# Optimization experiments

Measured on AMD Instinct MI355X. Metric: run time of the kernel, lower is better.

The kernel has to match this reference:

```python
import jax, jax.numpy as jnp
import numpy as np

D_MODEL = 1024


def setup_inputs() -> dict:
    key = jax.random.key(0)
    ks = jax.random.split(key, 7)
    s = 1.0 / np.sqrt(D_MODEL)
    return {
        "x": jax.random.normal(ks[0], (4, 4096, D_MODEL), dtype=jnp.float32),
        "Wq": jax.random.normal(ks[1], (D_MODEL, D_MODEL), dtype=jnp.float32) * s,
        "bq": jax.random.normal(ks[2], (D_MODEL,), dtype=jnp.float32) * s,
        "Wk": jax.random.normal(ks[3], (D_MODEL, D_MODEL), dtype=jnp.float32) * s,
        "bk": jax.random.normal(ks[4], (D_MODEL,), dtype=jnp.float32) * s,
        "Wv": jax.random.normal(ks[5], (D_MODEL, D_MODEL), dtype=jnp.float32) * s,
        "bv": jax.random.normal(ks[6], (D_MODEL,), dtype=jnp.float32) * s,
    }


def reference(x, Wq, bq, Wk, bk, Wv, bv):
    # nn.Linear: y = x @ W.T + b
    Q = jnp.einsum("bsd,ed->bse", x, Wq) + bq  # [B,S,D]
    K = jnp.einsum("bsd,ed->bse", x, Wk) + bk
    V = jnp.einsum("bsd,ed->bse", x, Wv) + bv
    scale = 1.0 / jnp.sqrt(jnp.asarray(x.shape[-1], dtype=x.dtype))
    KV = jnp.einsum("bsd,bse->bde", K, V) * scale  # [B,D,D]
    E = jnp.einsum("bsd,bde->bse", Q, KV)  # [B,S,D]
    return E
```

## Files before the change

### kernel.cpp

```cpp
#include <hip/hip_runtime.h>
#include <hip/hip_fp16.h>


#define BATCH 4
#define SEQ   4096
#define DM    1024

typedef _Float16 h8 __attribute__((ext_vector_type(8)));
typedef _Float16 h4 __attribute__((ext_vector_type(4)));
typedef float    f4 __attribute__((ext_vector_type(4)));

__device__ inline void gload_lds16(const _Float16* g, _Float16* l) {
    __builtin_amdgcn_global_load_lds(
        (const __attribute__((address_space(1))) void*)g,
        (__attribute__((address_space(3))) void*)l,
        16, 0, 0);
}

__device__ inline int xcd_swz(int bid, int grid) {
    const int q = grid >> 3;
    return (bid & 7) * q + (bid >> 3);
}

__device__ inline float doth(const _Float16* wr, const float* v, int lane) {
    float s = 0.f;
    #pragma unroll
    for (int i = 0; i < 2; ++i) {
        const int k = i * 512 + lane * 8;
        h8 wv = *(const h8*)&wr[k];
        f4 v0 = *(const f4*)&v[k];
        f4 v1 = *(const f4*)&v[k + 4];
        s += (float)wv[0] * v0.x + (float)wv[1] * v0.y +
             (float)wv[2] * v0.z + (float)wv[3] * v0.w +
             (float)wv[4] * v1.x + (float)wv[5] * v1.y +
             (float)wv[6] * v1.z + (float)wv[7] * v1.w;
    }
    return s;
}
__device__ inline float dotf(const float* a, const float* b, int lane) {
    float s = 0.f;
    #pragma unroll
    for (int i = 0; i < 4; ++i) {
        const int k = i * 256 + lane * 4;
        f4 x = *(const f4*)&a[k];
        f4 y = *(const f4*)&b[k];
        s += x.x * y.x + x.y * y.y + x.z * y.z + x.w * y.w;
    }
    return s;
}
__device__ inline float wred(float s) {
    #pragma unroll
    for (int off = 32; off; off >>= 1) s += __shfl_down(s, off);
    return s;
}

__global__ __launch_bounds__(256) void cvt_x(
    const float* __restrict__ src, _Float16* __restrict__ dstT,
    _Float16* __restrict__ dstRM, float* __restrict__ xs, int R, int C)
{
    __shared__ float tile[64][65];
    __shared__ float red[4][64];
    const long zoff = (long)blockIdx.z * R * C;
    src += zoff; dstT += zoff; dstRM += zoff;
    const int r0 = blockIdx.y * 64;
    const int c0 = blockIdx.x * 64;
    const int t  = threadIdx.x;
    const int tr = t >> 4;
    const int tc = (t & 15) * 4;
    #pragma unroll
    for (int i = 0; i < 4; ++i) {
        const int r = tr + i * 16;
        f4 v = *(const f4*)&src[(long)(r0 + r) * C + c0 + tc];
        tile[r][tc + 0] = v.x; tile[r][tc + 1] = v.y;
        tile[r][tc + 2] = v.z; tile[r][tc + 3] = v.w;
        h4 h = { (_Float16)v.x, (_Float16)v.y, (_Float16)v.z, (_Float16)v.w };
        *(h4*)&dstRM[(long)(r0 + r) * C + c0 + tc] = h;
    }
    __syncthreads();
    #pragma unroll
    for (int i = 0; i < 4; ++i) {
        const int c = tr + i * 16;
        h4 h = { (_Float16)tile[tc + 0][c], (_Float16)tile[tc + 1][c],
                 (_Float16)tile[tc + 2][c], (_Float16)tile[tc + 3][c] };
        *(h4*)&dstT[(long)(c0 + c) * R + r0 + tc] = h;
    }
    {
        const int cc = t & 63;
        const int rb = (t >> 6) * 16;
        float ps = 0.f;
        #pragma unroll
        for (int r = 0; r < 16; ++r) ps += tile[rb + r][cc];
        red[t >> 6][cc] = ps;
    }
    __syncthreads();
    if (t < 64)
        atomicAdd(&xs[blockIdx.z * DM + c0 + t],
                  red[0][t] + red[1][t] + red[2][t] + red[3][t]);
}

__global__ __launch_bounds__(256) void wcvt(
    const float* __restrict__ Wq, const float* __restrict__ Wk,
    const float* __restrict__ Wv,
    _Float16* __restrict__ Wqt, _Float16* __restrict__ Wkt,
    _Float16* __restrict__ Wkh, _Float16* __restrict__ Wvh)
{
    __shared__ float tile[64][65];
    const int z = blockIdx.z;
    const float* src = z == 0 ? Wq : (z == 1 ? Wk : Wv);
    _Float16* dstT  = z == 0 ? Wqt : (z == 1 ? Wkt : nullptr);
    _Float16* dstRM = z == 0 ? nullptr : (z == 1 ? Wkh : Wvh);
    const int r0 = blockIdx.y * 64;
    const int c0 = blockIdx.x * 64;
    const int t  = threadIdx.x;
    const int tr = t >> 4;
    const int tc = (t & 15) * 4;
    #pragma unroll
    for (int i = 0; i < 4; ++i) {
        const int r = tr + i * 16;
        f4 v = *(const f4*)&src[(long)(r0 + r) * DM + c0 + tc];
        tile[r][tc + 0] = v.x; tile[r][tc + 1] = v.y;
        tile[r][tc + 2] = v.z; tile[r][tc + 3] = v.w;
        if (dstRM) {
            h4 h = { (_Float16)v.x, (_Float16)v.y, (_Float16)v.z, (_Float16)v.w };
            *(h4*)&dstRM[(long)(r0 + r) * DM + c0 + tc] = h;
        }
    }
    __syncthreads();
    if (dstT) {
        #pragma unroll
        for (int i = 0; i < 4; ++i) {
            const int c = tr + i * 16;
            h4 h = { (_Float16)tile[tc + 0][c], (_Float16)tile[tc + 1][c],
                     (_Float16)tile[tc + 2][c], (_Float16)tile[tc + 3][c] };
            *(h4*)&dstT[(long)(c0 + c) * DM + r0 + tc] = h;
        }
    }
}

__global__ __launch_bounds__(256) void gemv_misc(
    const _Float16* __restrict__ Wvh, const _Float16* __restrict__ Wkh,
    const _Float16* __restrict__ Wqt, const _Float16* __restrict__ Wkt,
    const float* __restrict__ xs, const float* __restrict__ bv,
    const float* __restrict__ bk, const float* __restrict__ bq,
    float* __restrict__ vecs)
{
    const int gw   = blockIdx.x * 4 + (threadIdx.x >> 6);
    const int lane = threadIdx.x & 63;
    const _Float16* wr;
    const float* v;
    if (gw < 4096)      { wr = Wvh + (long)(gw & 1023) * DM; v = xs + (gw >> 10) * DM; }
    else if (gw < 8192) { wr = Wkh + (long)(gw & 1023) * DM; v = xs + ((gw - 4096) >> 10) * DM; }
    else if (gw < 9216) { wr = Wqt + (long)(gw - 8192) * DM; v = bk; }
    else                { wr = Wkt + (long)(gw - 9216) * DM; v = bq; }
    float s = wred(doth(wr, v, lane));
    if (lane == 0) {
        if (gw < 4096) s += (float)SEQ * bv[gw & 1023];
        vecs[gw] = s;
    }
}

__global__ __launch_bounds__(256) void gemv_qw(
    const _Float16* __restrict__ Wqt, const float* __restrict__ w,
    const float* __restrict__ bq, const float* __restrict__ bk,
    float* __restrict__ qw, float* __restrict__ sv)
{
    const int gw   = blockIdx.x * 4 + (threadIdx.x >> 6);
    const int lane = threadIdx.x & 63;
    if (gw < 4096) {
        float s = wred(doth(Wqt + (long)(gw & 1023) * DM, w + (gw >> 10) * DM, lane));
        if (lane == 0) qw[gw] = s;
    } else if (gw == 4096) {
        float s = wred(dotf(bq, bk, lane));
        if (lane == 0) sv[0] = s;
    } else if (gw <= 4100) {
        float s = wred(dotf(bq, w + (gw - 4097) * DM, lane));
        if (lane == 0) sv[1 + (gw - 4097)] = s;
    }
}

__global__ __launch_bounds__(256) void gemv_cv(
    const _Float16* __restrict__ Ph, const float* __restrict__ kb,
    const float* __restrict__ u2, const float* __restrict__ bv,
    const float* __restrict__ sv, float* __restrict__ cv)
{
    const int gw   = blockIdx.x * 4 + (threadIdx.x >> 6);
    const int lane = threadIdx.x & 63;
    const int b    = gw >> 10;
    const int e    = gw & 1023;
    float s = wred(doth(Ph + (long)b * DM * DM + (long)e * DM, kb, lane));
    if (lane == 0)
        cv[gw] = s + (sv[0] * u2[gw] + sv[1 + b] * bv[e]) * 0.03125f;
}

__global__ __launch_bounds__(256) void reduce_tri(
    const _Float16* __restrict__ parts, _Float16* __restrict__ Gh)
{
    __shared__ _Float16 lds[64][72];
    const int bid = blockIdx.x;
    const int job = bid >> 4;
    const int ch  = bid & 15;
    const int b   = job / 10;
    const int p   = job - b * 10;
    const int ti  = p >= 6 ? 3 : (p >= 3 ? 2 : (p >= 1 ? 1 : 0));
    const int tj  = p - ((ti * (ti + 1)) >> 1);
    const int li  = (ch >> 2) * 64;
    const int lj  = (ch & 3) * 64;
    const int t   = threadIdx.x;
    const int c8  = (t & 7) * 8;
    const long DD_ = (long)DM * DM;

    h8 o[2];
    #pragma unroll
    for (int h = 0; h < 2; ++h) {
        const int r = (t >> 3) + h * 32;
        float a[8] = {};
        #pragma unroll
        for (int s = 0; s < 6; ++s) {
            const _Float16* src = parts + ((long)(job * 6 + s) << 16);
            h8 v = *(const h8*)&src[(li + r) * 256 + lj + c8];
            #pragma unroll
            for (int j = 0; j < 8; ++j) a[j] += (float)v[j];
        }
        #pragma unroll
        for (int j = 0; j < 8; ++j) o[h][j] = (_Float16)(a[j] * 0.03125f);
        *(h8*)&Gh[b * DD_ + (long)(ti * 256 + li + r) * DM + tj * 256 + lj + c8] = o[h];
        *(h8*)&lds[r][c8] = o[h];
    }
    if (ti != tj) {
        __syncthreads();
        #pragma unroll
        for (int h = 0; h < 2; ++h) {
            const int r = (t >> 3) + h * 32;
            h8 m;
            #pragma unroll
            for (int j = 0; j < 8; ++j) m[j] = lds[c8 + j][r];
            *(h8*)&Gh[b * DD_ + (long)(tj * 256 + lj + r) * DM + ti * 256 + li + c8] = m;
        }
    }
}

template<typename OutT, int BIAS, int TRI>
__global__ __launch_bounds__(512, 1) void gemm8p(
    const _Float16* __restrict__ A, const _Float16* __restrict__ B,
    OutT* __restrict__ C,
    int K, int lda, int ldb, int ldc, int tilesX, int perZ,
    long aZ, long bZ, long cZ, int sk, long aK, long bK,
    const float* __restrict__ bc1, long bc1Z, float alpha)
{
    __shared__ _Float16 lds[2 * 32768];

    const int L = xcd_swz(blockIdx.x, gridDim.x);
    int tileM, tileN, cTileM, cTileN, NT;
    const float* pc1 = nullptr;
    if (TRI) {
        const int job = L / 6;
        const int s   = L - job * 6;
        const int b   = job / 10;
        const int p   = job - b * 10;
        const int ti  = p >= 6 ? 3 : (p >= 3 ? 2 : (p >= 1 ? 1 : 0));
        const int tj  = p - ((ti * (ti + 1)) >> 1);
        const int kOff = s < 4 ? s * 704 : 2816 + (s - 4) * 640;
        NT = s < 4 ? 11 : 10;
        A += (long)b * aZ + kOff;
        B += (long)b * aZ + kOff;
        C += (long)(job * 6 + s) * cZ;
        tileM = ti * 256; tileN = tj * 256;
        cTileM = 0; cTileN = 0;
    } else {
        const int z  = L / perZ;
        const int r0 = L - z * perZ;
        const int zb = z / sk;
        const int zk = z - zb * sk;
        A += (long)zb * aZ + (long)zk * aK;
        B += (long)zb * bZ + (long)zk * bK;
        C += (long)z * cZ;
        if (BIAS == 1) pc1 = bc1 + (long)zb * bc1Z;
        tileM = (r0 / tilesX) * 256;
        tileN = (r0 % tilesX) * 256;
        cTileM = tileM; cTileN = tileN;
        NT = K >> 6;
    }

    const int tid  = threadIdx.x;
    const int lane = tid & 63;
    const int wave = tid >> 6;
    const int wr   = wave >> 2;
    const int wc   = wave & 3;
    const int la   = lane & 15;
    const int kg   = lane >> 4;

    auto stageA = [&](int buf, int mq, int kt) {
        _Float16* dst = &lds[buf * 32768 + mq * 8192];
        const int k0 = kt * 64;
        #pragma unroll
        for (int i = 0; i < 2; ++i) {
            const int U = i * 512 + tid;
            const int R = U >> 3, s = U & 7;
            const int gr = tileM + (R >> 6) * 128 + mq * 64 + (R & 63);
            gload_lds16(&A[(long)gr * lda + k0 + ((s ^ (R & 7)) << 3)], dst + U * 8);
        }
    };
    auto stageB = [&](int buf, int nq, int kt) {
        _Float16* dst = &lds[buf * 32768 + 16384 + nq * 8192];
        const int k0 = kt * 64;
        #pragma unroll
        for (int i = 0; i < 2; ++i) {
            const int U = i * 512 + tid;
            const int R = U >> 3, s = U & 7;
            const int gn = tileN + (R >> 5) * 64 + nq * 32 + (R & 31);
            gload_lds16(&B[(long)gn * ldb + k0 + ((s ^ (R & 7)) << 3)], dst + U * 8);
        }
    };

    f4 acc[8][4] = {};
    h8 af[4][2];
    h8 bf[2][2][2];

    auto readA = [&](int buf, int mq) {
        const _Float16* Ab = &lds[buf * 32768 + mq * 8192];
        #pragma unroll
        for (int mi = 0; mi < 4; ++mi)
            #pragma unroll
            for (int kk = 0; kk < 2; ++kk) {
                const int R = wr * 64 + mi * 16 + la;
                const int s = kk * 4 + kg;
                af[mi][kk] = *(const h8*)&Ab[R * 64 + ((s ^ (R & 7)) << 3)];
            }
    };
    auto readB = [&](int buf, int nq) {
        const _Float16* Bb = &lds[buf * 32768 + 16384 + nq * 8192];
        #pragma unroll
        for (int ni = 0; ni < 2; ++ni)
            #pragma unroll
            for (int kk = 0; kk < 2; ++kk) {
                const int R = wc * 32 + ni * 16 + la;
                const int s = kk * 4 + kg;
                bf[nq][ni][kk] = *(const h8*)&Bb[R * 64 + ((s ^ (R & 7)) << 3)];
            }
    };
    auto mfmaQ = [&](int mq, int nq) {
        __builtin_amdgcn_s_setprio(1);
        #pragma unroll
        for (int mi = 0; mi < 4; ++mi)
            #pragma unroll
            for (int ni = 0; ni < 2; ++ni)
                #pragma unroll
                for (int kk = 0; kk < 2; ++kk)
                    acc[mq * 4 + mi][nq * 2 + ni] =
                        __builtin_amdgcn_mfma_f32_16x16x32_f16(
                            af[mi][kk], bf[nq][ni][kk],
                            acc[mq * 4 + mi][nq * 2 + ni], 0, 0, 0);
        __builtin_amdgcn_s_setprio(0);
    };

    stageA(0, 0, 0); stageA(0, 1, 0); stageB(0, 0, 0); stageB(0, 1, 0);
    if (NT > 1) {
        stageA(1, 0, 1); stageB(1, 0, 1);
        asm volatile("s_waitcnt vmcnt(4)" ::: "memory");
    } else {
        asm volatile("s_waitcnt vmcnt(0)" ::: "memory");
    }
    __builtin_amdgcn_sched_barrier(0);
    __builtin_amdgcn_s_barrier();

    for (int j = 0; j < NT; ++j) {
        const int buf = j & 1;
        readA(buf, 0); readB(buf, 0);
        if (j + 1 < NT) stageA(buf ^ 1, 1, j + 1);
        asm volatile("s_waitcnt lgkmcnt(8)" ::: "memory");
        __builtin_amdgcn_s_barrier();
        asm volatile("s_waitcnt lgkmcnt(0)" ::: "memory");
        __builtin_amdgcn_sched_barrier(0);
        mfmaQ(0, 0);
        __builtin_amdgcn_s_barrier();
        readB(buf, 1);
        if (j + 1 < NT) stageB(buf ^ 1, 1, j + 1);
        __builtin_amdgcn_s_barrier();
        asm volatile("s_waitcnt lgkmcnt(0)" ::: "memory");
        __builtin_amdgcn_sched_barrier(0);
        mfmaQ(0, 1);
        __builtin_amdgcn_s_barrier();
        readA(buf, 1);
        if (j + 2 < NT) stageA(buf, 0, j + 2);
        __builtin_amdgcn_s_barrier();
        asm volatile("s_waitcnt lgkmcnt(0)" ::: "memory");
        __builtin_amdgcn_sched_barrier(0);
        mfmaQ(1, 0);
        __builtin_amdgcn_s_barrier();
        if (j + 2 < NT) stageB(buf, 0, j + 2);
        __builtin_amdgcn_s_barrier();
        mfmaQ(1, 1);
        if (j + 2 < NT) {
            asm volatile("s_waitcnt vmcnt(4)" ::: "memory");
        } else if (j + 1 < NT) {
            asm volatile("s_waitcnt vmcnt(0)" ::: "memory");
        }
        __builtin_amdgcn_sched_barrier(0);
        __builtin_amdgcn_s_barrier();
    }

    #pragma unroll
    for (int mf = 0; mf < 8; ++mf) {
        #pragma unroll
        for (int nf = 0; nf < 4; ++nf) {
            const int col = cTileN + wc * 64 + nf * 16 + la;
            #pragma unroll
            for (int jj = 0; jj < 4; ++jj) {
                const int row = cTileM + wr * 128 + mf * 16 + kg * 4 + jj;
                float v = acc[mf][nf][jj] * alpha;
                if (BIAS == 1) v += pc1[col];
                C[(long)row * ldc + col] = (OutT)v;
            }
        }
    }
}

template<int BIAS>
__global__ __launch_bounds__(256) void gemm64(
    const _Float16* __restrict__ A, const _Float16* __restrict__ B,
    _Float16* __restrict__ C,
    const _Float16* __restrict__ A2, const _Float16* __restrict__ B2,
    _Float16* __restrict__ C2, int zSplit,
    int K, int lda, int ldb, int ldc, int tilesX, int perZ,
    long aZ, long bZ, long cZ,
    const float* __restrict__ bc1, long bc1Z,
    const float* __restrict__ br1, long br1Z,
    const float* __restrict__ bc2, long bc2Z,
    const float* __restrict__ br2, long br2Z,
    float alpha, float beta)
{
    __shared__ _Float16 As[64 * 64];
    __shared__ _Float16 Bs[64 * 64];

    const int L  = xcd_swz(blockIdx.x, gridDim.x);
    int z        = L / perZ;
    const int r0 = L - z * perZ;
    if (z >= zSplit) { A = A2; B = B2; C = C2; z = 0; }
    A += (long)z * aZ;
    B += (long)z * bZ;
    C += (long)z * cZ;
    const float* pc1 = nullptr; const float* pr1 = nullptr;
    const float* pc2 = nullptr; const float* pr2 = nullptr;
    if (BIAS == 3) {
        pc1 = bc1 + (long)z * bc1Z; pr1 = br1 + (long)z * br1Z;
        pc2 = bc2 + (long)z * bc2Z; pr2 = br2 + (long)z * br2Z;
    }

    const int tileM = (r0 / tilesX) * 64;
    const int tileN = (r0 % tilesX) * 64;
    const int tid   = threadIdx.x;
    const int lane  = tid & 63;
    const int wave  = tid >> 6;
    const int wm    = (wave >> 1) * 32;
    const int wn    = (wave & 1) * 32;
    const int srow  = tid >> 3;
    const int sslot = tid & 7;

    f4 acc[2][2] = {};
    const int arow = lane & 15;
    const int kg   = lane >> 4;

    for (int k0 = 0; k0 < K; k0 += 64) {
        #pragma unroll
        for (int i = 0; i < 2; ++i) {
            const int row   = i * 32 + srow;
            const int gslot = sslot ^ (row & 7);
            gload_lds16(&A[(long)(tileM + row) * lda + k0 + gslot * 8],
                        &As[row * 64 + sslot * 8]);
            gload_lds16(&B[(long)(tileN + row) * ldb + k0 + gslot * 8],
                        &Bs[row * 64 + sslot * 8]);
        }
        __syncthreads();

        #pragma unroll
        for (int kk = 0; kk < 64; kk += 32) {
            h8 af[2], bf[2];
            #pragma unroll
            for (int m = 0; m < 2; ++m) {
                const int rr   = wm + m * 16 + arow;
                const int slot = (kk >> 3) + kg;
                af[m] = *(const h8*)&As[rr * 64 + ((slot ^ (rr & 7)) << 3)];
            }
            #pragma unroll
            for (int n = 0; n < 2; ++n) {
                const int rr   = wn + n * 16 + arow;
                const int slot = (kk >> 3) + kg;
                bf[n] = *(const h8*)&Bs[rr * 64 + ((slot ^ (rr & 7)) << 3)];
            }
            #pragma unroll
            for (int m = 0; m < 2; ++m)
                #pragma unroll
                for (int n = 0; n < 2; ++n)
                    acc[m][n] = __builtin_amdgcn_mfma_f32_16x16x32_f16(
                        af[m], bf[n], acc[m][n], 0, 0, 0);
        }
        __syncthreads();
    }

    #pragma unroll
    for (int m = 0; m < 2; ++m) {
        #pragma unroll
        for (int n = 0; n < 2; ++n) {
            const int col = tileN + wn + n * 16 + arow;
            #pragma unroll
            for (int j = 0; j < 4; ++j) {
                const int row = tileM + wm + m * 16 + (lane >> 4) * 4 + j;
                float v = acc[m][n][j] * alpha;
                if (BIAS == 3) v += beta * (pc1[col] * pr1[row] + pc2[col] * pr2[row]);
                C[(long)row * ldc + col] = (_Float16)v;
            }
        }
    }
}

extern "C" void kernel_launch(void* const* d_in, const int* in_sizes, int n_in,
                              void* d_out, int out_size, void* d_ws, size_t ws_size,
                              hipStream_t stream)
{
    const float* x  = (const float*)d_in[0];
    const float* Wq = (const float*)d_in[1];
    const float* bq = (const float*)d_in[2];
    const float* Wk = (const float*)d_in[3];
    const float* bk = (const float*)d_in[4];
    const float* Wv = (const float*)d_in[5];
    const float* bv = (const float*)d_in[6];
    float* out = (float*)d_out;

    const long DD = (long)DM * DM;
    const long DS = (long)DM * SEQ;
    const long MB = 1024l * 1024;

    char* base = (char*)d_ws;
    _Float16* xh   = (_Float16*)base;
    _Float16* xt   = (_Float16*)(base + 32 * MB);
    _Float16* Gh   = xt;
    _Float16* Ph   = (_Float16*)(base + 40 * MB);
    _Float16* Rth  = (_Float16*)(base + 48 * MB);
    _Float16* Wqt  = (_Float16*)(base + 64 * MB);
    _Float16* Wkh  = (_Float16*)(base + 66 * MB);
    _Float16* Wvh  = (_Float16*)(base + 68 * MB);
    _Float16* Wkt  = (_Float16*)(base + 70 * MB);
    _Float16* Mh   = (_Float16*)(base + 72 * MB);
    float*    vecs = (float*)(base + 74 * MB);
    float*    u2   = vecs;
    float*    w    = vecs + 4096;
    float*    qk   = vecs + 8192;
    float*    kb   = vecs + 9216;
    float*    xs   = vecs + 10240;
    float*    qw   = vecs + 14336;
    float*    cv   = vecs + 18432;
    float*    sv   = vecs + 22528;
    _Float16* parts = (_Float16*)d_out;

    hipMemsetAsync(xs, 0, BATCH * DM * sizeof(float), stream);

    cvt_x<<<dim3(16, 64, 4), 256, 0, stream>>>(x, xt, xh, xs, SEQ, DM);
    wcvt<<<dim3(16, 16, 3), 256, 0, stream>>>(Wq, Wk, Wv, Wqt, Wkt, Wkh, Wvh);

    gemv_misc<<<2560, 256, 0, stream>>>(Wvh, Wkh, Wqt, Wkt, xs, bv, bk, bq, vecs);

    gemv_qw<<<1026, 256, 0, stream>>>(Wqt, w, bq, bk, qw, sv);

    gemm8p<_Float16, 0, 1><<<240, 512, 0, stream>>>(
        xt, xt, parts, 4096, SEQ, SEQ, 256, 0, 0,
        DS, DS, 65536, 1, 0, 0, nullptr, 0, 1.0f);

    reduce_tri<<<640, 256, 0, stream>>>(parts, Gh);

    gemm64<0><<<1280, 256, 0, stream>>>(
        Wvh, Gh, Ph, Wqt, Wkt, Mh, 4,
        1024, DM, DM, DM, 16, 256,
        0, DD, DD,
        nullptr, 0, nullptr, 0, nullptr, 0, nullptr, 0, 1.0f, 0.f);

    gemv_cv<<<1024, 256, 0, stream>>>(Ph, kb, u2, bv, sv, cv);

    gemm64<3><<<1024, 256, 0, stream>>>(
        Ph, Mh, Rth, nullptr, nullptr, nullptr, 99,
        1024, DM, DM, DM, 16, 256,
        DD, 0, DD,
        qk, 0, u2, 1024, qw, 1024, bv, 0, 1.0f, 0.03125f);

    gemm8p<float, 1, 0><<<256, 512, 0, stream>>>(
        xh, Rth, out, 1024, DM, DM, DM, 4, 64,
        DS, DD, DS, 1, 0, 0, cv, 1024, 1.0f);
}
```

Measured before the change: 156.9 us.

## Merge conversion kernels and reassociate small GEMVs to drop the Wk·xs pass

Merges the x and weight conversion kernels into one launch, so the separate Wk row-major fp16 copy is no longer written. The qw vector is now computed from the already-built Mh matrix times xs, instead of a two-step Wk·xs then Wqt product. The per-batch bias scalars become atomic accumulations of kb·xs. This removes two small kernel launches and one GEMV pass over a weight matrix. In exchange it adds atomics and relies on Mh being ready before the qw computation, which now runs after the Mh GEMM.

```diff
diff --git a/kernel.cpp b/kernel.cpp
--- a/kernel.cpp
+++ b/kernel.cpp
@@ -54,75 +54,54 @@
     return s;
 }
 
-__global__ __launch_bounds__(256) void cvt_x(
-    const float* __restrict__ src, _Float16* __restrict__ dstT,
-    _Float16* __restrict__ dstRM, float* __restrict__ xs, int R, int C)
+__global__ __launch_bounds__(256) void cvt_all(
+    const float* __restrict__ x, const float* __restrict__ Wq,
+    const float* __restrict__ Wk, const float* __restrict__ Wv,
+    _Float16* __restrict__ xt, _Float16* __restrict__ xh,
+    _Float16* __restrict__ Wqt, _Float16* __restrict__ Wkt,
+    _Float16* __restrict__ Wvh, float* __restrict__ xs)
 {
     __shared__ float tile[64][65];
     __shared__ float red[4][64];
-    const long zoff = (long)blockIdx.z * R * C;
-    src += zoff; dstT += zoff; dstRM += zoff;
-    const int r0 = blockIdx.y * 64;
-    const int c0 = blockIdx.x * 64;
-    const int t  = threadIdx.x;
-    const int tr = t >> 4;
-    const int tc = (t & 15) * 4;
+    const int bid = blockIdx.x;
+    const int t   = threadIdx.x;
+    const int tr  = t >> 4;
+    const int tc  = (t & 15) * 4;
+
+    const float* src;
+    _Float16 *dstT = nullptr, *dstRM = nullptr;
+    int r0, c0, C, R;
+    bool isX = bid < 4096;
+    if (isX) {
+        const int b  = bid >> 10;
+        const int tt = bid & 1023;
+        r0 = (tt >> 4) * 64; c0 = (tt & 15) * 64;
+        R = SEQ; C = DM;
+        src   = x  + (long)b * SEQ * DM;
+        dstT  = xt + (long)b * SEQ * DM;
+        dstRM = xh + (long)b * SEQ * DM;
+        xs   += b * DM;
+    } else {
+        const int wb = bid - 4096;
+        const int z  = wb >> 8;
+        const int tt = wb & 255;
+        r0 = (tt >> 4) * 64; c0 = (tt & 15) * 64;
+        R = DM; C = DM;
+        src = z == 0 ? Wq : (z == 1 ? Wk : Wv);
+        if (z == 0) dstT = Wqt;
+        else if (z == 1) dstT = Wkt;
+        else dstRM = Wvh;
+    }
+
     #pragma unroll
     for (int i = 0; i < 4; ++i) {
         const int r = tr + i * 16;
         f4 v = *(const f4*)&src[(long)(r0 + r) * C + c0 + tc];
         tile[r][tc + 0] = v.x; tile[r][tc + 1] = v.y;
         tile[r][tc + 2] = v.z; tile[r][tc + 3] = v.w;
-        h4 h = { (_Float16)v.x, (_Float16)v.y, (_Float16)v.z, (_Float16)v.w };
-        *(h4*)&dstRM[(long)(r0 + r) * C + c0 + tc] = h;
-    }
-    __syncthreads();
-    #pragma unroll
-    for (int i = 0; i < 4; ++i) {
-        const int c = tr + i * 16;
-        h4 h = { (_Float16)tile[tc + 0][c], (_Float16)tile[tc + 1][c],
-                 (_Float16)tile[tc + 2][c], (_Float16)tile[tc + 3][c] };
-        *(h4*)&dstT[(long)(c0 + c) * R + r0 + tc] = h;
-    }
-    {
-        const int cc = t & 63;
-        const int rb = (t >> 6) * 16;
-        float ps = 0.f;
-        #pragma unroll
-        for (int r = 0; r < 16; ++r) ps += tile[rb + r][cc];
-        red[t >> 6][cc] = ps;
-    }
-    __syncthreads();
-    if (t < 64)
-        atomicAdd(&xs[blockIdx.z * DM + c0 + t],
-                  red[0][t] + red[1][t] + red[2][t] + red[3][t]);
-}
-
-__global__ __launch_bounds__(256) void wcvt(
-    const float* __restrict__ Wq, const float* __restrict__ Wk,
-    const float* __restrict__ Wv,
-    _Float16* __restrict__ Wqt, _Float16* __restrict__ Wkt,
-    _Float16* __restrict__ Wkh, _Float16* __restrict__ Wvh)
-{
-    __shared__ float tile[64][65];
-    const int z = blockIdx.z;
-    const float* src = z == 0 ? Wq : (z == 1 ? Wk : Wv);
-    _Float16* dstT  = z == 0 ? Wqt : (z == 1 ? Wkt : nullptr);
-    _Float16* dstRM = z == 0 ? nullptr : (z == 1 ? Wkh : Wvh);
-    const int r0 = blockIdx.y * 64;
-    const int c0 = blockIdx.x * 64;
-    const int t  = threadIdx.x;
-    const int tr = t >> 4;
-    const int tc = (t & 15) * 4;
-    #pragma unroll
-    for (int i = 0; i < 4; ++i) {
-        const int r = tr + i * 16;
-        f4 v = *(const f4*)&src[(long)(r0 + r) * DM + c0 + tc];
-        tile[r][tc + 0] = v.x; tile[r][tc + 1] = v.y;
-        tile[r][tc + 2] = v.z; tile[r][tc + 3] = v.w;
         if (dstRM) {
             h4 h = { (_Float16)v.x, (_Float16)v.y, (_Float16)v.z, (_Float16)v.w };
-            *(h4*)&dstRM[(long)(r0 + r) * DM + c0 + tc] = h;
+            *(h4*)&dstRM[(long)(r0 + r) * C + c0 + tc] = h;
         }
     }
     __syncthreads();
@@ -132,64 +111,75 @@
             const int c = tr + i * 16;
             h4 h = { (_Float16)tile[tc + 0][c], (_Float16)tile[tc + 1][c],
                      (_Float16)tile[tc + 2][c], (_Float16)tile[tc + 3][c] };
-            *(h4*)&dstT[(long)(c0 + c) * DM + r0 + tc] = h;
-        }
+            *(h4*)&dstT[(long)(c0 + c) * R + r0 + tc] = h;
+        }
+    }
+    if (isX) {
+        const int cc = t & 63;
+        const int rb = (t >> 6) * 16;
+        float ps = 0.f;
+        #pragma unroll
+        for (int r = 0; r < 16; ++r) ps += tile[rb + r][cc];
+        red[t >> 6][cc] = ps;
+        __syncthreads();
+        if (t < 64)
+            atomicAdd(&xs[c0 + t], red[0][t] + red[1][t] + red[2][t] + red[3][t]);
     }
 }
 
 __global__ __launch_bounds__(256) void gemv_misc(
-    const _Float16* __restrict__ Wvh, const _Float16* __restrict__ Wkh,
-    const _Float16* __restrict__ Wqt, const _Float16* __restrict__ Wkt,
+    const _Float16* __restrict__ Wvh, const _Float16* __restrict__ Wqt,
+    const _Float16* __restrict__ Wkt,
     const float* __restrict__ xs, const float* __restrict__ bv,
     const float* __restrict__ bk, const float* __restrict__ bq,
-    float* __restrict__ vecs)
-{
-    const int gw   = blockIdx.x * 4 + (threadIdx.x >> 6);
-    const int lane = threadIdx.x & 63;
-    const _Float16* wr;
-    const float* v;
-    if (gw < 4096)      { wr = Wvh + (long)(gw & 1023) * DM; v = xs + (gw >> 10) * DM; }
-    else if (gw < 8192) { wr = Wkh + (long)(gw & 1023) * DM; v = xs + ((gw - 4096) >> 10) * DM; }
-    else if (gw < 9216) { wr = Wqt + (long)(gw - 8192) * DM; v = bk; }
-    else                { wr = Wkt + (long)(gw - 9216) * DM; v = bq; }
-    float s = wred(doth(wr, v, lane));
-    if (lane == 0) {
-        if (gw < 4096) s += (float)SEQ * bv[gw & 1023];
-        vecs[gw] = s;
-    }
-}
-
-__global__ __launch_bounds__(256) void gemv_qw(
-    const _Float16* __restrict__ Wqt, const float* __restrict__ w,
-    const float* __restrict__ bq, const float* __restrict__ bk,
-    float* __restrict__ qw, float* __restrict__ sv)
+    float* __restrict__ u2, float* __restrict__ qk,
+    float* __restrict__ kb, float* __restrict__ sv)
 {
     const int gw   = blockIdx.x * 4 + (threadIdx.x >> 6);
     const int lane = threadIdx.x & 63;
     if (gw < 4096) {
-        float s = wred(doth(Wqt + (long)(gw & 1023) * DM, w + (gw >> 10) * DM, lane));
-        if (lane == 0) qw[gw] = s;
-    } else if (gw == 4096) {
+        float s = wred(doth(Wvh + (long)(gw & 1023) * DM, xs + (gw >> 10) * DM, lane));
+        if (lane == 0) u2[gw] = s + (float)SEQ * bv[gw & 1023];
+    } else if (gw < 5120) {
+        float s = wred(doth(Wqt + (long)(gw - 4096) * DM, bk, lane));
+        if (lane == 0) qk[gw - 4096] = s;
+    } else if (gw < 6144) {
+        const int j = gw - 5120;
+        float s = wred(doth(Wkt + (long)j * DM, bq, lane));
+        if (lane == 0) {
+            kb[j] = s;
+            #pragma unroll
+            for (int b = 0; b < 4; ++b)
+                atomicAdd(&sv[1 + b], s * xs[b * DM + j]);
+        }
+    } else if (gw == 6144) {
         float s = wred(dotf(bq, bk, lane));
         if (lane == 0) sv[0] = s;
-    } else if (gw <= 4100) {
-        float s = wred(dotf(bq, w + (gw - 4097) * DM, lane));
-        if (lane == 0) sv[1 + (gw - 4097)] = s;
-    }
-}
-
-__global__ __launch_bounds__(256) void gemv_cv(
-    const _Float16* __restrict__ Ph, const float* __restrict__ kb,
+    }
+}
+
+__global__ __launch_bounds__(256) void gemv_cvqw(
+    const _Float16* __restrict__ Ph, const _Float16* __restrict__ Mh,
+    const float* __restrict__ kb, const float* __restrict__ xs,
     const float* __restrict__ u2, const float* __restrict__ bv,
-    const float* __restrict__ sv, float* __restrict__ cv)
+    const float* __restrict__ sv,
+    float* __restrict__ cv, float* __restrict__ qw)
 {
     const int gw   = blockIdx.x * 4 + (threadIdx.x >> 6);
     const int lane = threadIdx.x & 63;
-    const int b    = gw >> 10;
-    const int e    = gw & 1023;
-    float s = wred(doth(Ph + (long)b * DM * DM + (long)e * DM, kb, lane));
-    if (lane == 0)
-        cv[gw] = s + (sv[0] * u2[gw] + sv[1 + b] * bv[e]) * 0.03125f;
+    if (gw < 4096) {
+        const int b = gw >> 10;
+        const int e = gw & 1023;
+        float s = wred(doth(Ph + (long)b * DM * DM + (long)e * DM, kb, lane));
+        if (lane == 0)
+            cv[gw] = s + (sv[0] * u2[gw] + sv[1 + b] * bv[e]) * 0.03125f;
+    } else {
+        const int g = gw - 4096;
+        const int b = g >> 10;
+        const int i = g & 1023;
+        float s = wred(doth(Mh + (long)i * DM, xs + b * DM, lane));
+        if (lane == 0) qw[g] = s;
+    }
 }
 
 __global__ __launch_bounds__(256) void reduce_tri(
@@ -537,29 +527,24 @@
     _Float16* Ph   = (_Float16*)(base + 40 * MB);
     _Float16* Rth  = (_Float16*)(base + 48 * MB);
     _Float16* Wqt  = (_Float16*)(base + 64 * MB);
-    _Float16* Wkh  = (_Float16*)(base + 66 * MB);
-    _Float16* Wvh  = (_Float16*)(base + 68 * MB);
-    _Float16* Wkt  = (_Float16*)(base + 70 * MB);
-    _Float16* Mh   = (_Float16*)(base + 72 * MB);
-    float*    vecs = (float*)(base + 74 * MB);
+    _Float16* Wvh  = (_Float16*)(base + 66 * MB);
+    _Float16* Wkt  = (_Float16*)(base + 68 * MB);
+    _Float16* Mh   = (_Float16*)(base + 70 * MB);
+    float*    vecs = (float*)(base + 72 * MB);
     float*    u2   = vecs;
-    float*    w    = vecs + 4096;
-    float*    qk   = vecs + 8192;
-    float*    kb   = vecs + 9216;
-    float*    xs   = vecs + 10240;
-    float*    qw   = vecs + 14336;
-    float*    cv   = vecs + 18432;
-    float*    sv   = vecs + 22528;
+    float*    qk   = vecs + 4096;
+    float*    kb   = vecs + 5120;
+    float*    xs   = vecs + 6144;
+    float*    qw   = vecs + 10240;
+    float*    cv   = vecs + 14336;
+    float*    sv   = vecs + 18432;
     _Float16* parts = (_Float16*)d_out;
 
-    hipMemsetAsync(xs, 0, BATCH * DM * sizeof(float), stream);
-
-    cvt_x<<<dim3(16, 64, 4), 256, 0, stream>>>(x, xt, xh, xs, SEQ, DM);
-    wcvt<<<dim3(16, 16, 3), 256, 0, stream>>>(Wq, Wk, Wv, Wqt, Wkt, Wkh, Wvh);
-
-    gemv_misc<<<2560, 256, 0, stream>>>(Wvh, Wkh, Wqt, Wkt, xs, bv, bk, bq, vecs);
-
-    gemv_qw<<<1026, 256, 0, stream>>>(Wqt, w, bq, bk, qw, sv);
+    hipMemsetAsync(vecs, 0, 18440 * sizeof(float), stream);
+
+    cvt_all<<<4864, 256, 0, stream>>>(x, Wq, Wk, Wv, xt, xh, Wqt, Wkt, Wvh, xs);
+
+    gemv_misc<<<1537, 256, 0, stream>>>(Wvh, Wqt, Wkt, xs, bv, bk, bq, u2, qk, kb, sv);
 
     gemm8p<_Float16, 0, 1><<<240, 512, 0, stream>>>(
         xt, xt, parts, 4096, SEQ, SEQ, 256, 0, 0,
@@ -573,7 +558,7 @@
         0, DD, DD,
         nullptr, 0, nullptr, 0, nullptr, 0, nullptr, 0, 1.0f, 0.f);
 
-    gemv_cv<<<1024, 256, 0, stream>>>(Ph, kb, u2, bv, sv, cv);
+    gemv_cvqw<<<2048, 256, 0, stream>>>(Ph, Mh, kb, xs, u2, bv, sv, cv, qw);
 
     gemm64<3><<<1024, 256, 0, stream>>>(
         Ph, Mh, Rth, nullptr, nullptr, nullptr, 99,
```

After: 201.0 us. 1.28x slower.
